# Kernel tuning notes

Hardware: AMD Instinct MI355X
Metric: run time of the kernel (lower is better)

The kernel has to match this reference:

```python
import jax, jax.numpy as jnp
import numpy as np

BATCH_K = 4  # matches init_kwargs batch_k
B, D = 8192, 128

def setup_inputs() -> dict:
    key = jax.random.key(0)
    x = jax.random.normal(key, (B, D), dtype=jnp.float32)
    return {"x": x}

def _losses(x):
    b = x.shape[0]
    k = BATCH_K
    # Pairwise squared distances via Gram matrix: d2[i,j] = ||x_i - x_j||^2
    sq = jnp.sum(x * x, axis=-1)                      # [B]
    d2 = sq[:, None] + sq[None, :] - 2.0 * (x @ x.T)  # [B, B]
    g = jnp.arange(b) // k                            # group id per row
    same = g[:, None] == g[None, :]
    homo_mask = same & ~jnp.eye(b, dtype=bool)        # same group, i != j
    heter_mask = g[:, None] < g[None, :]              # anchor group strictly before j's group
    cnt_homo = jnp.asarray((b // k) * k * (k - 1), dtype=x.dtype)
    cnt_heter = jnp.sum(heter_mask).astype(x.dtype)
    loss_homo = jnp.sum(jnp.where(homo_mask, d2, 0.0)) / cnt_homo
    loss_heter = jnp.sum(jnp.where(heter_mask, jnp.maximum(1.0 - d2, 0.0), 0.0)) / cnt_heter
    return loss_homo, loss_heter

def reference(x):
    return _losses(x)
```

## Files before the change

kernel.cpp:

```cpp
#include <hip/hip_runtime.h>


#define DIM   128
#define NBT   32
#define NTRI  528
#define NPREP 512

typedef __bf16 bf16x8 __attribute__((ext_vector_type(8)));
typedef float  f32x16 __attribute__((ext_vector_type(16)));

__device__ __forceinline__ unsigned short f2bf(float f) {
  unsigned int u = __float_as_uint(f);
  u += 0x7fffu + ((u >> 16) & 1u);
  return (unsigned short)(u >> 16);
}

__device__ __forceinline__ float wave_reduce(float v) {
#pragma unroll
  for (int off = 32; off > 0; off >>= 1) v += __shfl_xor(v, off);
  return v;
}

__device__ __forceinline__ void load_lds16(const void* g, void* l) {
  __builtin_amdgcn_global_load_lds(
      (const __attribute__((address_space(1))) void*)g,
      (__attribute__((address_space(3))) void*)l, 16, 0, 0);
}

__global__ __launch_bounds__(256) void prep_kernel(
    const float* __restrict__ x, unsigned short* __restrict__ xb,
    float* __restrict__ sq, float* __restrict__ homo_part) {
  const int wave = threadIdx.x >> 6;
  const int lane = threadIdx.x & 63;
  const int g = blockIdx.x * 4 + wave;
  float s0 = 0.f, s1 = 0.f, q = 0.f;
#pragma unroll
  for (int r = 0; r < 4; ++r) {
    const int row = g * 4 + r;
    const float v0 = x[row * DIM + lane];
    const float v1 = x[row * DIM + lane + 64];
    s0 += v0; s1 += v1;
    float rq = wave_reduce(v0 * v0 + v1 * v1);
    if (lane == 0) sq[row] = rq;
    q += rq;
  }
  float ss = wave_reduce(s0 * s0 + s1 * s1);
  __shared__ float hred[4];
  if (lane == 0) hred[wave] = 8.f * q - 2.f * ss;

  const int r = lane >> 4, s = lane & 15;
  const int row = g * 4 + r;
  const int c = s ^ (row & 15);
  const float4* px = (const float4*)(x + row * DIM + c * 8);
  const float4 u0 = px[0], u1 = px[1];
  unsigned int p0 = (unsigned)f2bf(u0.x) | ((unsigned)f2bf(u0.y) << 16);
  unsigned int p1 = (unsigned)f2bf(u0.z) | ((unsigned)f2bf(u0.w) << 16);
  unsigned int p2 = (unsigned)f2bf(u1.x) | ((unsigned)f2bf(u1.y) << 16);
  unsigned int p3 = (unsigned)f2bf(u1.z) | ((unsigned)f2bf(u1.w) << 16);
  uint4 pk; pk.x = p0; pk.y = p1; pk.z = p2; pk.w = p3;
  *(uint4*)(xb + row * DIM + s * 8) = pk;

  __syncthreads();
  if (threadIdx.x == 0)
    homo_part[blockIdx.x] = hred[0] + hred[1] + hred[2] + hred[3];
}

__global__ __launch_bounds__(512, 2) void heter_kernel(
    const unsigned short* __restrict__ xb, const float* __restrict__ sq,
    float* __restrict__ partial) {
  __shared__ unsigned short ldsA[256 * DIM];
  __shared__ unsigned short ldsB[256 * DIM];

  const int t = (blockIdx.x & 7) * (NTRI / 8) + (blockIdx.x >> 3);
  int bi = (int)((65.0f - sqrtf(4225.0f - 8.0f * (float)t)) * 0.5f);
  bi = min(max(bi, 0), NBT - 1);
  while ((bi + 1) * NBT - ((bi + 1) * bi) / 2 <= t) ++bi;
  while (bi * NBT - (bi * (bi - 1)) / 2 > t) --bi;
  const int bj = bi + (t - (bi * NBT - (bi * (bi - 1)) / 2));

  const int wave = threadIdx.x >> 6;
  const int lane = threadIdx.x & 63;
  const bool diagBlock = (bi == bj);

  const unsigned short* gA = xb + bi * 256 * DIM;
  const unsigned short* gB = xb + bj * 256 * DIM;
#pragma unroll
  for (int i = 0; i < 8; ++i) {
    const int e = (wave * 32 + i * 4) * DIM;
    load_lds16(gA + e + lane * 8, &ldsA[e]);
    if (!diagBlock) load_lds16(gB + e + lane * 8, &ldsB[e]);
  }
  __syncthreads();
  const unsigned short* ldsBr = diagBlock ? ldsA : ldsB;

  const int wi = wave >> 2, wj = wave & 3;
  const int lc = lane & 31;
  const int lk = lane >> 5;
  const int sl = lc & 15;

  float hs = 0.f;
  if (!(diagBlock && (wj + 1) * 64 <= wi * 128)) {
    f32x16 acc[4][2];
#pragma unroll
    for (int a = 0; a < 4; ++a)
#pragma unroll
      for (int b = 0; b < 2; ++b)
#pragma unroll
        for (int v = 0; v < 16; ++v) acc[a][b][v] = 0.f;

#pragma unroll
    for (int ks = 0; ks < 8; ++ks) {
      const int so = ((ks * 2 + lk) ^ sl) * 8;
      bf16x8 a0 = *(const bf16x8*)&ldsA[(wi * 128 +  0 + lc) * DIM + so];
      bf16x8 a1 = *(const bf16x8*)&ldsA[(wi * 128 + 32 + lc) * DIM + so];
      bf16x8 a2 = *(const bf16x8*)&ldsA[(wi * 128 + 64 + lc) * DIM + so];
      bf16x8 a3 = *(const bf16x8*)&ldsA[(wi * 128 + 96 + lc) * DIM + so];
      bf16x8 b0 = *(const bf16x8*)&ldsBr[(wj * 64 +  0 + lc) * DIM + so];
      bf16x8 b1 = *(const bf16x8*)&ldsBr[(wj * 64 + 32 + lc) * DIM + so];
      acc[0][0] = __builtin_amdgcn_mfma_f32_32x32x16_bf16(a0, b0, acc[0][0], 0, 0, 0);
      acc[0][1] = __builtin_amdgcn_mfma_f32_32x32x16_bf16(a0, b1, acc[0][1], 0, 0, 0);
      acc[1][0] = __builtin_amdgcn_mfma_f32_32x32x16_bf16(a1, b0, acc[1][0], 0, 0, 0);
      acc[1][1] = __builtin_amdgcn_mfma_f32_32x32x16_bf16(a1, b1, acc[1][1], 0, 0, 0);
      acc[2][0] = __builtin_amdgcn_mfma_f32_32x32x16_bf16(a2, b0, acc[2][0], 0, 0, 0);
      acc[2][1] = __builtin_amdgcn_mfma_f32_32x32x16_bf16(a2, b1, acc[2][1], 0, 0, 0);
      acc[3][0] = __builtin_amdgcn_mfma_f32_32x32x16_bf16(a3, b0, acc[3][0], 0, 0, 0);
      acc[3][1] = __builtin_amdgcn_mfma_f32_32x32x16_bf16(a3, b1, acc[3][1], 0, 0, 0);
    }

    const int rbase = bi * 256 + wi * 128;
    const int cbase = bj * 256 + wj * 64;
    float cj0 = 1.f - sq[cbase + lc];
    float cj1 = 1.f - sq[cbase + 32 + lc];
#pragma unroll
    for (int fi = 0; fi < 4; ++fi) {
      const int frow = wi * 128 + fi * 32;
#pragma unroll
      for (int r = 0; r < 16; ++r) {
        const int io = (r & 3) + 8 * (r >> 2) + 4 * lk;
        const int i = rbase + fi * 32 + io;
        const float si = sq[i];
#pragma unroll
        for (int fj = 0; fj < 2; ++fj) {
          const int fcol = wj * 64 + fj * 32;
          if (diagBlock && fcol < frow) continue;
          float h = fmaxf(fmaf(2.f, acc[fi][fj][r], (fj ? cj1 : cj0) - si), 0.f);
          if (diagBlock && fcol == frow) {
            const int j = cbase + fj * 32 + lc;
            if (!((i >> 2) < (j >> 2))) h = 0.f;
          }
          hs += h;
        }
      }
    }
  }

  hs = wave_reduce(hs);
  __shared__ float red[8];
  if (lane == 0) red[wave] = hs;
  __syncthreads();
  if (threadIdx.x == 0) {
    float bsum = 0.f;
#pragma unroll
    for (int w = 0; w < 8; ++w) bsum += red[w];
    partial[t] = bsum;
  }
}

__global__ __launch_bounds__(256) void finalize_kernel(
    const float* __restrict__ partial, const float* __restrict__ homo_part,
    float* __restrict__ out) {
  float s = 0.f, hmo = 0.f;
  for (int i = threadIdx.x; i < NTRI; i += 256) s += partial[i];
  for (int i = threadIdx.x; i < NPREP; i += 256) hmo += homo_part[i];
  s = wave_reduce(s);
  hmo = wave_reduce(hmo);
  __shared__ float red[4], hred[4];
  const int wave = threadIdx.x >> 6, lane = threadIdx.x & 63;
  if (lane == 0) { red[wave] = s; hred[wave] = hmo; }
  __syncthreads();
  if (threadIdx.x == 0) {
    out[0] = (hred[0] + hred[1] + hred[2] + hred[3]) / 24576.f;
    out[1] = (red[0] + red[1] + red[2] + red[3]) / 33538048.f;
  }
}

extern "C" void kernel_launch(void* const* d_in, const int* in_sizes, int n_in,
                              void* d_out, int out_size, void* d_ws, size_t ws_size,
                              hipStream_t stream) {
  const float* x = (const float*)d_in[0];
  float* out = (float*)d_out;
  char* ws = (char*)d_ws;
  float* homo_part   = (float*)(ws);
  float* partial     = (float*)(ws + 2048);
  float* sq          = (float*)(ws + 10496);
  unsigned short* xb = (unsigned short*)(ws + 43264);

  hipLaunchKernelGGL(prep_kernel, dim3(NPREP), dim3(256), 0, stream, x, xb, sq, homo_part);
  hipLaunchKernelGGL(heter_kernel, dim3(NTRI), dim3(512), 0, stream, xb, sq, partial);
  hipLaunchKernelGGL(finalize_kernel, dim3(1), dim3(256), 0, stream, partial, homo_part, out);
}
```

Before: 96.98 us.

## Restructure heter GEMM into 128x64 jobs with register-resident A and double-buffered B

Replaces the 256x256 triangular tiles (528 blocks of 512 threads) with 4160 upper-triangle 128x64 jobs spread over 1024 blocks of 256 threads. Each block keeps its A-fragment in registers and streams B tiles through a double-buffered LDS pipeline, prefetching the next tile while computing the current one. The aim is to cut wasted work on diagonal tiles, shrink LDS use so more blocks fit per CU, and overlap global loads with MFMA. The trade-off is less reuse per loaded B tile, an A reload whenever the row strip changes, and a barrier on every job.

```diff
diff --git a/kernel.cpp b/kernel.cpp
--- a/kernel.cpp
+++ b/kernel.cpp
@@ -2,8 +2,8 @@
 
 
 #define DIM   128
-#define NBT   32
-#define NTRI  528
+#define NJOB  4160
+#define NBLK  1024
 #define NPREP 512
 
 typedef __bf16 bf16x8 __attribute__((ext_vector_type(8)));
@@ -48,9 +48,9 @@
   __shared__ float hred[4];
   if (lane == 0) hred[wave] = 8.f * q - 2.f * ss;
 
-  const int r = lane >> 4, s = lane & 15;
+  const int r = lane >> 4, sl = lane & 15;
   const int row = g * 4 + r;
-  const int c = s ^ (row & 15);
+  const int c = sl ^ (row & 15);
   const float4* px = (const float4*)(x + row * DIM + c * 8);
   const float4 u0 = px[0], u1 = px[1];
   unsigned int p0 = (unsigned)f2bf(u0.x) | ((unsigned)f2bf(u0.y) << 16);
@@ -58,119 +58,137 @@
   unsigned int p2 = (unsigned)f2bf(u1.x) | ((unsigned)f2bf(u1.y) << 16);
   unsigned int p3 = (unsigned)f2bf(u1.z) | ((unsigned)f2bf(u1.w) << 16);
   uint4 pk; pk.x = p0; pk.y = p1; pk.z = p2; pk.w = p3;
-  *(uint4*)(xb + row * DIM + s * 8) = pk;
+  *(uint4*)(xb + row * DIM + sl * 8) = pk;
 
   __syncthreads();
   if (threadIdx.x == 0)
     homo_part[blockIdx.x] = hred[0] + hred[1] + hred[2] + hred[3];
 }
 
-__global__ __launch_bounds__(512, 2) void heter_kernel(
+__global__ __launch_bounds__(256, 4) void heter_kernel(
     const unsigned short* __restrict__ xb, const float* __restrict__ sq,
     float* __restrict__ partial) {
-  __shared__ unsigned short ldsA[256 * DIM];
-  __shared__ unsigned short ldsB[256 * DIM];
-
-  const int t = (blockIdx.x & 7) * (NTRI / 8) + (blockIdx.x >> 3);
-  int bi = (int)((65.0f - sqrtf(4225.0f - 8.0f * (float)t)) * 0.5f);
-  bi = min(max(bi, 0), NBT - 1);
-  while ((bi + 1) * NBT - ((bi + 1) * bi) / 2 <= t) ++bi;
-  while (bi * NBT - (bi * (bi - 1)) / 2 > t) --bi;
-  const int bj = bi + (t - (bi * NBT - (bi * (bi - 1)) / 2));
+  __shared__ unsigned short Bl[2][64 * DIM];
 
   const int wave = threadIdx.x >> 6;
   const int lane = threadIdx.x & 63;
-  const bool diagBlock = (bi == bj);
-
-  const unsigned short* gA = xb + bi * 256 * DIM;
-  const unsigned short* gB = xb + bj * 256 * DIM;
-#pragma unroll
-  for (int i = 0; i < 8; ++i) {
-    const int e = (wave * 32 + i * 4) * DIM;
-    load_lds16(gA + e + lane * 8, &ldsA[e]);
-    if (!diagBlock) load_lds16(gB + e + lane * 8, &ldsB[e]);
-  }
-  __syncthreads();
-  const unsigned short* ldsBr = diagBlock ? ldsA : ldsB;
-
-  const int wi = wave >> 2, wj = wave & 3;
   const int lc = lane & 31;
   const int lk = lane >> 5;
   const int sl = lc & 15;
 
+  const int x = blockIdx.x & 7, u = blockIdx.x >> 3;
+  int j = x * 520 + 4 * u + min(u, 8);
+  const int jend = j + ((u < 8) ? 5 : 4);
+
+  int s = (int)((129.0f - sqrtf(16641.0f - 4.0f * (float)j)) * 0.5f);
+  s = min(max(s, 0), 63);
+  while ((s + 1) * (129 - (s + 1)) <= j) ++s;
+  while (s * (129 - s) > j) --s;
+  int c = j - s * (129 - s);
+
+  bf16x8 a[8];
+  {
+    const unsigned short* pA = xb + (128 * s + 32 * wave + lc) * DIM;
+#pragma unroll
+    for (int ks = 0; ks < 8; ++ks)
+      a[ks] = *(const bf16x8*)(pA + (((2 * ks + lk) ^ sl) << 3));
+  }
+
+  {
+    const unsigned short* g = xb + (128 * s + 64 * c) * DIM;
+#pragma unroll
+    for (int i = 0; i < 4; ++i) {
+      const int e = (wave * 16 + i * 4) * DIM;
+      load_lds16(g + e + lane * 8, &Bl[0][e]);
+    }
+  }
+
+  int buf = 0;
   float hs = 0.f;
-  if (!(diagBlock && (wj + 1) * 64 <= wi * 128)) {
-    f32x16 acc[4][2];
-#pragma unroll
-    for (int a = 0; a < 4; ++a)
-#pragma unroll
-      for (int b = 0; b < 2; ++b)
-#pragma unroll
-        for (int v = 0; v < 16; ++v) acc[a][b][v] = 0.f;
-
+  while (j < jend) {
+    __syncthreads();
+
+    const int nj = j + 1;
+    int ns = s, nc = c + 1;
+    const bool havenext = (nj < jend);
+    if (havenext) {
+      if (nc >= 128 - 2 * ns) { ++ns; nc = 0; }
+      const unsigned short* g = xb + (128 * ns + 64 * nc) * DIM;
+#pragma unroll
+      for (int i = 0; i < 4; ++i) {
+        const int e = (wave * 16 + i * 4) * DIM;
+        load_lds16(g + e + lane * 8, &Bl[buf ^ 1][e]);
+      }
+    }
+
+    const unsigned short* bl = &Bl[buf][0];
+    f32x16 acc0, acc1;
+#pragma unroll
+    for (int v = 0; v < 16; ++v) { acc0[v] = 0.f; acc1[v] = 0.f; }
 #pragma unroll
     for (int ks = 0; ks < 8; ++ks) {
-      const int so = ((ks * 2 + lk) ^ sl) * 8;
-      bf16x8 a0 = *(const bf16x8*)&ldsA[(wi * 128 +  0 + lc) * DIM + so];
-      bf16x8 a1 = *(const bf16x8*)&ldsA[(wi * 128 + 32 + lc) * DIM + so];
-      bf16x8 a2 = *(const bf16x8*)&ldsA[(wi * 128 + 64 + lc) * DIM + so];
-      bf16x8 a3 = *(const bf16x8*)&ldsA[(wi * 128 + 96 + lc) * DIM + so];
-      bf16x8 b0 = *(const bf16x8*)&ldsBr[(wj * 64 +  0 + lc) * DIM + so];
-      bf16x8 b1 = *(const bf16x8*)&ldsBr[(wj * 64 + 32 + lc) * DIM + so];
-      acc[0][0] = __builtin_amdgcn_mfma_f32_32x32x16_bf16(a0, b0, acc[0][0], 0, 0, 0);
-      acc[0][1] = __builtin_amdgcn_mfma_f32_32x32x16_bf16(a0, b1, acc[0][1], 0, 0, 0);
-      acc[1][0] = __builtin_amdgcn_mfma_f32_32x32x16_bf16(a1, b0, acc[1][0], 0, 0, 0);
-      acc[1][1] = __builtin_amdgcn_mfma_f32_32x32x16_bf16(a1, b1, acc[1][1], 0, 0, 0);
-      acc[2][0] = __builtin_amdgcn_mfma_f32_32x32x16_bf16(a2, b0, acc[2][0], 0, 0, 0);
-      acc[2][1] = __builtin_amdgcn_mfma_f32_32x32x16_bf16(a2, b1, acc[2][1], 0, 0, 0);
-      acc[3][0] = __builtin_amdgcn_mfma_f32_32x32x16_bf16(a3, b0, acc[3][0], 0, 0, 0);
-      acc[3][1] = __builtin_amdgcn_mfma_f32_32x32x16_bf16(a3, b1, acc[3][1], 0, 0, 0);
-    }
-
-    const int rbase = bi * 256 + wi * 128;
-    const int cbase = bj * 256 + wj * 64;
-    float cj0 = 1.f - sq[cbase + lc];
-    float cj1 = 1.f - sq[cbase + 32 + lc];
-#pragma unroll
-    for (int fi = 0; fi < 4; ++fi) {
-      const int frow = wi * 128 + fi * 32;
+      const int so = (((2 * ks + lk) ^ sl) << 3);
+      bf16x8 vb0 = *(const bf16x8*)&bl[(lc) * DIM + so];
+      bf16x8 vb1 = *(const bf16x8*)&bl[(32 + lc) * DIM + so];
+      acc0 = __builtin_amdgcn_mfma_f32_32x32x16_bf16(a[ks], vb0, acc0, 0, 0, 0);
+      acc1 = __builtin_amdgcn_mfma_f32_32x32x16_bf16(a[ks], vb1, acc1, 0, 0, 0);
+    }
+
+    {
+      const int fr = 32 * wave;
+      const int cb = 128 * s + 64 * c;
+      const int rb = 128 * s + fr;
+      const bool up0 = (64 * c >= fr), dg0 = (64 * c == fr);
+      const bool up1 = (64 * c + 32 >= fr), dg1 = (64 * c + 32 == fr);
+      const float cj0 = 1.f - sq[cb + lc];
+      const float cj1 = 1.f - sq[cb + 32 + lc];
+      const int jg0 = (cb + lc) >> 2, jg1 = (cb + 32 + lc) >> 2;
 #pragma unroll
       for (int r = 0; r < 16; ++r) {
         const int io = (r & 3) + 8 * (r >> 2) + 4 * lk;
-        const int i = rbase + fi * 32 + io;
+        const int i = rb + io;
+        const int ig = i >> 2;
         const float si = sq[i];
-#pragma unroll
-        for (int fj = 0; fj < 2; ++fj) {
-          const int fcol = wj * 64 + fj * 32;
-          if (diagBlock && fcol < frow) continue;
-          float h = fmaxf(fmaf(2.f, acc[fi][fj][r], (fj ? cj1 : cj0) - si), 0.f);
-          if (diagBlock && fcol == frow) {
-            const int j = cbase + fj * 32 + lc;
-            if (!((i >> 2) < (j >> 2))) h = 0.f;
-          }
+        if (up0) {
+          float h = fmaxf(fmaf(2.f, acc0[r], cj0 - si), 0.f);
+          if (dg0 && !(ig < jg0)) h = 0.f;
+          hs += h;
+        }
+        if (up1) {
+          float h = fmaxf(fmaf(2.f, acc1[r], cj1 - si), 0.f);
+          if (dg1 && !(ig < jg1)) h = 0.f;
           hs += h;
         }
       }
     }
+
+    if (havenext) {
+      if (ns != s) {
+        s = ns;
+        const unsigned short* pA = xb + (128 * s + 32 * wave + lc) * DIM;
+#pragma unroll
+        for (int ks = 0; ks < 8; ++ks)
+          a[ks] = *(const bf16x8*)(pA + (((2 * ks + lk) ^ sl) << 3));
+      }
+      c = nc;
+      buf ^= 1;
+    }
+    j = nj;
   }
 
   hs = wave_reduce(hs);
-  __shared__ float red[8];
+  __shared__ float red[4];
   if (lane == 0) red[wave] = hs;
   __syncthreads();
-  if (threadIdx.x == 0) {
-    float bsum = 0.f;
-#pragma unroll
-    for (int w = 0; w < 8; ++w) bsum += red[w];
-    partial[t] = bsum;
-  }
+  if (threadIdx.x == 0)
+    partial[blockIdx.x] = red[0] + red[1] + red[2] + red[3];
 }
 
 __global__ __launch_bounds__(256) void finalize_kernel(
     const float* __restrict__ partial, const float* __restrict__ homo_part,
     float* __restrict__ out) {
   float s = 0.f, hmo = 0.f;
-  for (int i = threadIdx.x; i < NTRI; i += 256) s += partial[i];
+  for (int i = threadIdx.x; i < NBLK; i += 256) s += partial[i];
   for (int i = threadIdx.x; i < NPREP; i += 256) hmo += homo_part[i];
   s = wave_reduce(s);
   hmo = wave_reduce(hmo);
@@ -196,6 +214,6 @@
   unsigned short* xb = (unsigned short*)(ws + 43264);
 
   hipLaunchKernelGGL(prep_kernel, dim3(NPREP), dim3(256), 0, stream, x, xb, sq, homo_part);
-  hipLaunchKernelGGL(heter_kernel, dim3(NTRI), dim3(512), 0, stream, xb, sq, partial);
+  hipLaunchKernelGGL(heter_kernel, dim3(NBLK), dim3(256), 0, stream, xb, sq, partial);
   hipLaunchKernelGGL(finalize_kernel, dim3(1), dim3(256), 0, stream, partial, homo_part, out);
 }
```

Result: faster. 79.58 us (-17.9%).
